# Performance work log

Hardware: AMD Instinct MI355X
Metric: run time of the kernel (lower is better)

## Reference

```python
import jax, jax.numpy as jnp
import numpy as np

HEADS = 16
DIM_HEAD = 64
SCALE = DIM_HEAD ** -0.5
LN_EPS = 1e-5


def setup_inputs() -> dict:
    key = jax.random.key(0)
    k1, k2, k3 = jax.random.split(key, 3)
    b, s, d = 2, 2048, 1024
    inner = HEADS * DIM_HEAD
    x = jax.random.normal(k1, (b, s, d), dtype=jnp.float32)
    w_qkv = jax.random.normal(k2, (d, 3 * inner), dtype=jnp.float32) * (d ** -0.5)
    w_out = jax.random.normal(k3, (inner, d), dtype=jnp.float32) * (inner ** -0.5)
    return {
        "x": x,
        "ln_gamma": jnp.ones((d,), jnp.float32),
        "ln_beta": jnp.zeros((d,), jnp.float32),
        "w_qkv": w_qkv,
        "w_out": w_out,
        "b_out": jnp.zeros((d,), jnp.float32),
    }


def _layernorm(x, gamma, beta):
    mu = jnp.mean(x, axis=-1, keepdims=True)
    var = jnp.var(x, axis=-1, keepdims=True)
    return (x - mu) * jax.lax.rsqrt(var + LN_EPS) * gamma + beta


def reference(x, ln_gamma, ln_beta, w_qkv, w_out, b_out):
    b, s, d = x.shape
    xn = _layernorm(x, ln_gamma, ln_beta)
    qkv = xn @ w_qkv                       # [b, s, 3*inner]
    q, k, v = jnp.split(qkv, 3, axis=-1)
    def heads(t):
        return t.reshape(b, s, HEADS, DIM_HEAD).transpose(0, 2, 1, 3)  # [b, h, s, dh]
    q, k, v = heads(q), heads(k), heads(v)
    dots = jnp.einsum("bhqd,bhkd->bhqk", q, k) * SCALE   # [b, h, s, s]
    attn = jax.nn.softmax(dots, axis=-1)
    out = jnp.einsum("bhqk,bhkd->bhqd", attn, v)          # [b, h, s, dh]
    out = out.transpose(0, 2, 1, 3).reshape(b, s, HEADS * DIM_HEAD)
    return out @ w_out + b_out
```

## Files before the change

### kernel.cpp

```cpp
#include <hip/hip_runtime.h>
#include <hip/hip_bf16.h>
#include <stdint.h>

#define NH     16
#define DHEAD  64
#define SEQ    2048
#define DMODEL 1024
#define NBATCH 2
#define INNER  1024
#define QKVN   3072
#define ROWS   4096
#define ATT_QB 64
#define ATT_KB 64

typedef __attribute__((ext_vector_type(8))) __bf16 bf16x8;
typedef __attribute__((ext_vector_type(4))) float floatx4;

__device__ __forceinline__ unsigned short f2bf(float f) {
    union { __bf16 b; unsigned short u; } c; c.b = (__bf16)f; return c.u;
}

__device__ __forceinline__ float fexp2(float x) {
#if __has_builtin(__builtin_amdgcn_exp2f)
    return __builtin_amdgcn_exp2f(x);
#else
    float r; asm("v_exp_f32 %0, %1" : "=v"(r) : "v"(x)); return r;
#endif
}

typedef __attribute__((address_space(1))) void gvoid;
typedef __attribute__((address_space(3))) void lvoid;
__device__ __forceinline__ void gl_lds16(const void* g, void* l) {
    __builtin_amdgcn_global_load_lds((gvoid*)g, (lvoid*)l, 16, 0, 0);
}

__global__ __launch_bounds__(256) void transpose_f2b(
        const float* __restrict__ in, unsigned short* __restrict__ out,
        int rows, int cols) {
    __shared__ unsigned short tile[32][33];
    const int bx = blockIdx.x * 32, by = blockIdx.y * 32;
    const int tx = threadIdx.x & 31, ty = threadIdx.x >> 5;
    for (int i = ty; i < 32; i += 8)
        tile[i][tx] = f2bf(in[(size_t)(by + i) * cols + bx + tx]);
    __syncthreads();
    for (int i = ty; i < 32; i += 8)
        out[(size_t)(bx + i) * rows + by + tx] = tile[tx][i];
}

__global__ __launch_bounds__(256) void ln_kernel(
        const float* __restrict__ x,
        const float* __restrict__ gamma,
        const float* __restrict__ beta,
        unsigned short* __restrict__ xn) {
    __shared__ float red[4][2];
    const int row = blockIdx.x, t = threadIdx.x;
    const size_t base = (size_t)row * DMODEL + t * 4;
    float4 v = *(const float4*)(x + base);
    float s  = v.x + v.y + v.z + v.w;
    float ss = v.x*v.x + v.y*v.y + v.z*v.z + v.w*v.w;
    for (int off = 32; off >= 1; off >>= 1) {
        s  += __shfl_xor(s,  off);
        ss += __shfl_xor(ss, off);
    }
    const int w = t >> 6, lane = t & 63;
    if (lane == 0) { red[w][0] = s; red[w][1] = ss; }
    __syncthreads();
    if (t == 0) {
        float S  = red[0][0] + red[1][0] + red[2][0] + red[3][0];
        float SS = red[0][1] + red[1][1] + red[2][1] + red[3][1];
        float mu  = S * (1.f / DMODEL);
        float var = SS * (1.f / DMODEL) - mu * mu;
        red[0][0] = mu; red[0][1] = rsqrtf(var + 1e-5f);
    }
    __syncthreads();
    const float mu = red[0][0], rstd = red[0][1];
    float4 g = *(const float4*)(gamma + t * 4);
    float4 bb = *(const float4*)(beta + t * 4);
    ushort4 o;
    o.x = f2bf((v.x - mu) * rstd * g.x + bb.x);
    o.y = f2bf((v.y - mu) * rstd * g.y + bb.y);
    o.z = f2bf((v.z - mu) * rstd * g.z + bb.z);
    o.w = f2bf((v.w - mu) * rstd * g.w + bb.w);
    *(ushort4*)(xn + base) = o;
}

__global__ __launch_bounds__(256) void gemm_qkv(
        const unsigned short* __restrict__ A,
        const unsigned short* __restrict__ Bt,
        unsigned short* __restrict__ qP,
        unsigned short* __restrict__ kP,
        unsigned short* __restrict__ vT) {
    const int K = DMODEL;
    __shared__ __align__(16) unsigned short sA[128 * 32];
    __shared__ __align__(16) unsigned short sB[128 * 32];
    __shared__ __align__(16) unsigned short tb[2][64 * 72];
    const int t = threadIdx.x;
    const int mBase = blockIdx.y * 128, nBase = blockIdx.x * 128;
    const int w = t >> 6, lane = t & 63, quad = lane >> 4, l16 = lane & 15;
    const int wm = (w >> 1) * 64, wn = (w & 1) * 64;
    const int srow = t >> 2, sch = t & 3;
    floatx4 acc[4][4];
    for (int mi = 0; mi < 4; mi++)
        for (int ni = 0; ni < 4; ni++) acc[mi][ni] = (floatx4)0.f;

    for (int k0 = 0; k0 < K; k0 += 32) {
        #pragma unroll
        for (int c = 0; c < 2; c++) {
            const int row = c * 64 + srow;
            const int gcol = (sch ^ ((row >> 1) & 3)) * 8;
            gl_lds16(&A[(size_t)(mBase + row) * K + k0 + gcol], &sA[(c * 256 + w * 64) * 8]);
            gl_lds16(&Bt[(size_t)(nBase + row) * K + k0 + gcol], &sB[(c * 256 + w * 64) * 8]);
        }
        __syncthreads();
        bf16x8 af[4], bfv[4];
        #pragma unroll
        for (int mi = 0; mi < 4; mi++) {
            const int r = wm + mi * 16 + l16;
            af[mi] = *(const bf16x8*)&sA[r * 32 + (quad ^ ((r >> 1) & 3)) * 8];
        }
        #pragma unroll
        for (int ni = 0; ni < 4; ni++) {
            const int r = wn + ni * 16 + l16;
            bfv[ni] = *(const bf16x8*)&sB[r * 32 + (quad ^ ((r >> 1) & 3)) * 8];
        }
        #pragma unroll
        for (int mi = 0; mi < 4; mi++)
            #pragma unroll
            for (int ni = 0; ni < 4; ni++)
                acc[mi][ni] = __builtin_amdgcn_mfma_f32_16x16x32_bf16(
                    af[mi], bfv[ni], acc[mi][ni], 0, 0, 0);
        __syncthreads();
    }
    const int reg = nBase >> 10;
    if (reg == 2) {
        #pragma unroll
        for (int ni = 0; ni < 4; ni++) {
            const int col = nBase + wn + ni * 16 + l16;
            const int h = (col & 1023) >> 6, dh = col & 63;
            #pragma unroll
            for (int mi = 0; mi < 4; mi++) {
                const int row0 = mBase + wm + mi * 16 + quad * 4;
                const int b = row0 >> 11, s0 = row0 & 2047;
                ushort4 o;
                o.x = f2bf(acc[mi][ni][0]); o.y = f2bf(acc[mi][ni][1]);
                o.z = f2bf(acc[mi][ni][2]); o.w = f2bf(acc[mi][ni][3]);
                *(ushort4*)&vT[((size_t)(b * NH + h) * DHEAD + dh) * SEQ + s0] = o;
            }
        }
    } else {
        unsigned short* dst = (reg == 0) ? qP : kP;
        const float scl = (reg == 0) ? 0.18033688011112042f : 1.f;
        const int hh = ((nBase + wn) & 1023) >> 6;
        #pragma unroll
        for (int ph = 0; ph < 2; ph++) {
            if ((w >> 1) == ph) {
                unsigned short* tb_ = &tb[w & 1][0];
                #pragma unroll
                for (int mi = 0; mi < 4; mi++)
                    #pragma unroll
                    for (int ni = 0; ni < 4; ni++)
                        #pragma unroll
                        for (int i = 0; i < 4; i++)
                            tb_[(mi * 16 + quad * 4 + i) * 72 + ni * 16 + l16] =
                                f2bf(acc[mi][ni][i] * scl);
                asm volatile("s_waitcnt lgkmcnt(0)" ::: "memory");
                const int row_g = mBase + wm + lane;
                const int b = row_g >> 11, sr = row_g & 2047;
                unsigned short* orow = dst + ((size_t)(b * NH + hh) * SEQ + sr) * DHEAD;
                #pragma unroll
                for (int c = 0; c < 8; c++)
                    *(bf16x8*)&orow[c * 8] = *(const bf16x8*)&tb_[lane * 72 + c * 8];
            }
            __syncthreads();
        }
    }
}

__global__ __launch_bounds__(256) void gemm_out(
        const unsigned short* __restrict__ A,
        const unsigned short* __restrict__ Bt,
        float* __restrict__ C,
        const int M, const int N, const int K,
        const float* __restrict__ bias) {
    __shared__ __align__(16) unsigned short sA[128 * 32];
    __shared__ __align__(16) unsigned short sB[64 * 32];
    const int t = threadIdx.x;
    const int mBase = blockIdx.y * 128, nBase = blockIdx.x * 64;
    const int w = t >> 6, lane = t & 63, quad = lane >> 4, l16 = lane & 15;
    const int wm = (w >> 1) * 64, wn = (w & 1) * 32;
    const int srow = t >> 2, sch = t & 3;
    floatx4 acc[4][2];
    for (int mi = 0; mi < 4; mi++)
        for (int ni = 0; ni < 2; ni++) acc[mi][ni] = (floatx4)0.f;

    for (int k0 = 0; k0 < K; k0 += 32) {
        #pragma unroll
        for (int c = 0; c < 2; c++) {
            const int row = c * 64 + srow;
            const int gcol = (sch ^ ((row >> 1) & 3)) * 8;
            gl_lds16(&A[(size_t)(mBase + row) * K + k0 + gcol], &sA[(c * 256 + w * 64) * 8]);
        }
        {
            const int gcol = (sch ^ ((srow >> 1) & 3)) * 8;
            gl_lds16(&Bt[(size_t)(nBase + srow) * K + k0 + gcol], &sB[(w * 64) * 8]);
        }
        __syncthreads();
        bf16x8 af[4], bfv[2];
        #pragma unroll
        for (int mi = 0; mi < 4; mi++) {
            const int r = wm + mi * 16 + l16;
            af[mi] = *(const bf16x8*)&sA[r * 32 + (quad ^ ((r >> 1) & 3)) * 8];
        }
        #pragma unroll
        for (int ni = 0; ni < 2; ni++) {
            const int r = wn + ni * 16 + l16;
            bfv[ni] = *(const bf16x8*)&sB[r * 32 + (quad ^ ((r >> 1) & 3)) * 8];
        }
        #pragma unroll
        for (int mi = 0; mi < 4; mi++)
            #pragma unroll
            for (int ni = 0; ni < 2; ni++)
                acc[mi][ni] = __builtin_amdgcn_mfma_f32_16x16x32_bf16(
                    af[mi], bfv[ni], acc[mi][ni], 0, 0, 0);
        __syncthreads();
    }
    #pragma unroll
    for (int mi = 0; mi < 4; mi++)
        #pragma unroll
        for (int ni = 0; ni < 2; ni++) {
            const int col = nBase + wn + ni * 16 + l16;
            const float badd = bias ? bias[col] : 0.f;
            #pragma unroll
            for (int i = 0; i < 4; i++) {
                const int row = mBase + wm + mi * 16 + quad * 4 + i;
                C[(size_t)row * N + col] = acc[mi][ni][i] + badd;
            }
        }
}

__global__ __launch_bounds__(256, 4) void attn_kernel(
        const unsigned short* __restrict__ qP,
        const unsigned short* __restrict__ kP,
        const unsigned short* __restrict__ vT,
        unsigned short* __restrict__ aout) {
    __shared__ __align__(16) unsigned short sK[2][ATT_KB * 64];
    __shared__ __align__(16) unsigned short sV[2][ATT_KB * 64];
    __shared__ __align__(16) unsigned short sP[4][16 * 64];
    const int t = threadIdx.x, w = t >> 6, lane = t & 63;
    const int quad = lane >> 4, l16 = lane & 15;
    const int bid = blockIdx.x;
    const int xcd = bid & 7, slot = bid >> 3;
    const int bh = xcd * 4 + (slot >> 5);
    const int qb = slot & 31;
    const int b = bh >> 4, h = bh & 15;
    const int qbase = qb * ATT_QB + w * 16;
    const int swr = l16 & 7;

    bf16x8 aq[2];
    #pragma unroll
    for (int hh = 0; hh < 2; hh++)
        aq[hh] = *(const bf16x8*)&qP[
            ((size_t)bh * SEQ + qbase + l16) * DHEAD + hh * 32 + quad * 8];

    floatx4 oac[4];
    float lS = 0.f;
    #pragma unroll
    for (int c = 0; c < 4; c++) oac[c] = (floatx4)0.f;

    const unsigned short* kb = kP + (size_t)bh * SEQ * DHEAD;
    const unsigned short* vb = vT + (size_t)bh * DHEAD * SEQ;
    const int r8 = lane >> 3, sw8 = ((lane & 7) ^ r8) * 8;

    auto stage = [&](int it, int bi) {
        const int kv0 = it * ATT_KB;
        #pragma unroll
        for (int ii = 0; ii < 2; ii++) {
            const int row = w * 16 + ii * 8 + r8;
            gl_lds16(kb + (size_t)(kv0 + row) * DHEAD + sw8,
                     (void*)&sK[bi][(w * 16 + ii * 8) * 64]);
            gl_lds16(vb + (size_t)row * SEQ + kv0 + sw8,
                     (void*)&sV[bi][(w * 16 + ii * 8) * 64]);
        }
    };
    stage(0, 0);

    const int NIT = SEQ / ATT_KB;
    for (int it = 0; it < NIT; ++it) {
        __syncthreads();
        if (it + 1 < NIT) stage(it + 1, (it + 1) & 1);
        const unsigned short* sKb = &sK[it & 1][0];
        const unsigned short* sVb = &sV[it & 1][0];

        bf16x8 kf[4][2];
        #pragma unroll
        for (int c = 0; c < 4; c++)
            #pragma unroll
            for (int hh = 0; hh < 2; hh++)
                kf[c][hh] = *(const bf16x8*)&sKb[(c * 16 + l16) * 64 +
                                                 8 * (((hh << 2) | quad) ^ swr)];
        floatx4 sv[4];
        __builtin_amdgcn_s_setprio(1);
        #pragma unroll
        for (int c = 0; c < 4; c++) {
            floatx4 a = (floatx4)0.f;
            a = __builtin_amdgcn_mfma_f32_16x16x32_bf16(kf[c][0], aq[0], a, 0, 0, 0);
            a = __builtin_amdgcn_mfma_f32_16x16x32_bf16(kf[c][1], aq[1], a, 0, 0, 0);
            sv[c] = a;
        }
        __builtin_amdgcn_s_setprio(0);
        {
            float sum = 0.f;
            unsigned short* pb = (unsigned short*)&sP[w][0];
            #pragma unroll
            for (int c = 0; c < 4; c++) {
                float p0 = fexp2(sv[c][0]), p1 = fexp2(sv[c][1]);
                float p2 = fexp2(sv[c][2]), p3 = fexp2(sv[c][3]);
                sum += (p0 + p1) + (p2 + p3);
                ushort4 pk;
                pk.x = f2bf(p0); pk.y = f2bf(p1); pk.z = f2bf(p2); pk.w = f2bf(p3);
                *(ushort4*)&pb[l16 * 64 + 8 * ((((c << 1) | (quad >> 1))) ^ swr) + (quad & 1) * 4] = pk;
            }
            sum += __shfl_xor(sum, 16);
            sum += __shfl_xor(sum, 32);
            lS += sum;
        }
        bf16x8 vf[4][2];
        #pragma unroll
        for (int c = 0; c < 4; c++)
            #pragma unroll
            for (int hh = 0; hh < 2; hh++)
                vf[c][hh] = *(const bf16x8*)&sVb[(c * 16 + l16) * 64 +
                                                 8 * (((hh << 2) | quad) ^ swr)];
        asm volatile("s_waitcnt lgkmcnt(0)" ::: "memory");
        {
            const unsigned short* pb = (const unsigned short*)&sP[w][0];
            bf16x8 pf[2];
            #pragma unroll
            for (int hh = 0; hh < 2; hh++)
                pf[hh] = *(const bf16x8*)&pb[l16 * 64 + 8 * (((hh << 2) | quad) ^ swr)];
            __builtin_amdgcn_s_setprio(1);
            #pragma unroll
            for (int c = 0; c < 4; c++) {
                oac[c] = __builtin_amdgcn_mfma_f32_16x16x32_bf16(vf[c][0], pf[0], oac[c], 0, 0, 0);
                oac[c] = __builtin_amdgcn_mfma_f32_16x16x32_bf16(vf[c][1], pf[1], oac[c], 0, 0, 0);
            }
            __builtin_amdgcn_s_setprio(0);
        }
    }
    const float rl = 1.f / lS;
    unsigned short* orow = aout + ((size_t)(b * SEQ + qbase + l16)) * INNER + h * DHEAD;
    #pragma unroll
    for (int c = 0; c < 4; c++) {
        ushort4 o;
        o.x = f2bf(oac[c][0] * rl);
        o.y = f2bf(oac[c][1] * rl);
        o.z = f2bf(oac[c][2] * rl);
        o.w = f2bf(oac[c][3] * rl);
        *(ushort4*)&orow[c * 16 + quad * 4] = o;
    }
}

extern "C" void kernel_launch(void* const* d_in, const int* in_sizes, int n_in,
                              void* d_out, int out_size, void* d_ws, size_t ws_size,
                              hipStream_t stream) {
    const float* x     = (const float*)d_in[0];
    const float* gamma = (const float*)d_in[1];
    const float* beta  = (const float*)d_in[2];
    const float* wqkv  = (const float*)d_in[3];
    const float* wout  = (const float*)d_in[4];
    const float* bout  = (const float*)d_in[5];
    float* out = (float*)d_out;

    unsigned short* ws     = (unsigned short*)d_ws;
    unsigned short* xn     = ws;
    unsigned short* wqkvT  = xn     + (size_t)ROWS * DMODEL;
    unsigned short* qPb    = wqkvT  + (size_t)QKVN * DMODEL;
    unsigned short* kPb    = qPb    + (size_t)NBATCH * NH * SEQ * DHEAD;
    unsigned short* vTb    = kPb    + (size_t)NBATCH * NH * SEQ * DHEAD;
    unsigned short* attnO  = vTb    + (size_t)NBATCH * NH * SEQ * DHEAD;
    unsigned short* woutT  = attnO  + (size_t)ROWS * INNER;

    transpose_f2b<<<dim3(QKVN / 32, DMODEL / 32), 256, 0, stream>>>(wqkv, wqkvT, DMODEL, QKVN);
    transpose_f2b<<<dim3(DMODEL / 32, INNER / 32), 256, 0, stream>>>(wout, woutT, INNER, DMODEL);
    ln_kernel<<<ROWS, 256, 0, stream>>>(x, gamma, beta, xn);
    gemm_qkv<<<dim3(QKVN / 128, ROWS / 128), 256, 0, stream>>>(xn, wqkvT, qPb, kPb, vTb);
    attn_kernel<<<dim3((SEQ / ATT_QB) * NBATCH * NH), 256, 0, stream>>>(
        qPb, kPb, vTb, attnO);
    gemm_out<<<dim3(DMODEL / 64, ROWS / 128), 256, 0, stream>>>(
        attnO, woutT, out, ROWS, DMODEL, INNER, bout);
}
```

Measured before the change: 216.4 us.

## Process two query sub-tiles per wave in attention with 128-thread blocks

The attention kernel now runs 2 waves per block instead of 4, and each wave handles 32 query rows as two 16-row sub-tiles. K and V fragments loaded from LDS are reused across both sub-tiles, which halves LDS fragment reads per unit of MFMA work, and each wave stages more rows of the K/V tile. The cost is higher register pressure from doubled accumulators and Q fragments, and fewer waves per block to hide latency, with launch bounds set to (128,2).

```diff
diff --git a/kernel.cpp b/kernel.cpp
--- a/kernel.cpp
+++ b/kernel.cpp
@@ -238,14 +238,14 @@
         }
 }
 
-__global__ __launch_bounds__(256, 4) void attn_kernel(
+__global__ __launch_bounds__(128, 2) void attn_kernel(
         const unsigned short* __restrict__ qP,
         const unsigned short* __restrict__ kP,
         const unsigned short* __restrict__ vT,
         unsigned short* __restrict__ aout) {
     __shared__ __align__(16) unsigned short sK[2][ATT_KB * 64];
     __shared__ __align__(16) unsigned short sV[2][ATT_KB * 64];
-    __shared__ __align__(16) unsigned short sP[4][16 * 64];
+    __shared__ __align__(16) unsigned short sP[2][2][16 * 64];
     const int t = threadIdx.x, w = t >> 6, lane = t & 63;
     const int quad = lane >> 4, l16 = lane & 15;
     const int bid = blockIdx.x;
@@ -253,19 +253,23 @@
     const int bh = xcd * 4 + (slot >> 5);
     const int qb = slot & 31;
     const int b = bh >> 4, h = bh & 15;
-    const int qbase = qb * ATT_QB + w * 16;
+    const int qbase = qb * ATT_QB + w * 32;
     const int swr = l16 & 7;
 
-    bf16x8 aq[2];
+    bf16x8 aq[2][2];
     #pragma unroll
-    for (int hh = 0; hh < 2; hh++)
-        aq[hh] = *(const bf16x8*)&qP[
-            ((size_t)bh * SEQ + qbase + l16) * DHEAD + hh * 32 + quad * 8];
-
-    floatx4 oac[4];
-    float lS = 0.f;
+    for (int st = 0; st < 2; st++)
+        #pragma unroll
+        for (int hh = 0; hh < 2; hh++)
+            aq[st][hh] = *(const bf16x8*)&qP[
+                ((size_t)bh * SEQ + qbase + st * 16 + l16) * DHEAD + hh * 32 + quad * 8];
+
+    floatx4 oac[2][4];
+    float lS[2] = {0.f, 0.f};
     #pragma unroll
-    for (int c = 0; c < 4; c++) oac[c] = (floatx4)0.f;
+    for (int st = 0; st < 2; st++)
+        #pragma unroll
+        for (int c = 0; c < 4; c++) oac[st][c] = (floatx4)0.f;
 
     const unsigned short* kb = kP + (size_t)bh * SEQ * DHEAD;
     const unsigned short* vb = vT + (size_t)bh * DHEAD * SEQ;
@@ -274,12 +278,12 @@
     auto stage = [&](int it, int bi) {
         const int kv0 = it * ATT_KB;
         #pragma unroll
-        for (int ii = 0; ii < 2; ii++) {
-            const int row = w * 16 + ii * 8 + r8;
+        for (int ii = 0; ii < 4; ii++) {
+            const int row = w * 32 + ii * 8 + r8;
             gl_lds16(kb + (size_t)(kv0 + row) * DHEAD + sw8,
-                     (void*)&sK[bi][(w * 16 + ii * 8) * 64]);
+                     (void*)&sK[bi][(w * 32 + ii * 8) * 64]);
             gl_lds16(vb + (size_t)row * SEQ + kv0 + sw8,
-                     (void*)&sV[bi][(w * 16 + ii * 8) * 64]);
+                     (void*)&sV[bi][(w * 32 + ii * 8) * 64]);
         }
     };
     stage(0, 0);
@@ -298,23 +302,26 @@
             for (int hh = 0; hh < 2; hh++)
                 kf[c][hh] = *(const bf16x8*)&sKb[(c * 16 + l16) * 64 +
                                                  8 * (((hh << 2) | quad) ^ swr)];
-        floatx4 sv[4];
+        floatx4 sv[2][4];
         __builtin_amdgcn_s_setprio(1);
         #pragma unroll
-        for (int c = 0; c < 4; c++) {
-            floatx4 a = (floatx4)0.f;
-            a = __builtin_amdgcn_mfma_f32_16x16x32_bf16(kf[c][0], aq[0], a, 0, 0, 0);
-            a = __builtin_amdgcn_mfma_f32_16x16x32_bf16(kf[c][1], aq[1], a, 0, 0, 0);
-            sv[c] = a;
-        }
+        for (int st = 0; st < 2; st++)
+            #pragma unroll
+            for (int c = 0; c < 4; c++) {
+                floatx4 a = (floatx4)0.f;
+                a = __builtin_amdgcn_mfma_f32_16x16x32_bf16(kf[c][0], aq[st][0], a, 0, 0, 0);
+                a = __builtin_amdgcn_mfma_f32_16x16x32_bf16(kf[c][1], aq[st][1], a, 0, 0, 0);
+                sv[st][c] = a;
+            }
         __builtin_amdgcn_s_setprio(0);
-        {
+        #pragma unroll
+        for (int st = 0; st < 2; st++) {
             float sum = 0.f;
-            unsigned short* pb = (unsigned short*)&sP[w][0];
+            unsigned short* pb = (unsigned short*)&sP[w][st][0];
             #pragma unroll
             for (int c = 0; c < 4; c++) {
-                float p0 = fexp2(sv[c][0]), p1 = fexp2(sv[c][1]);
-                float p2 = fexp2(sv[c][2]), p3 = fexp2(sv[c][3]);
+                float p0 = fexp2(sv[st][c][0]), p1 = fexp2(sv[st][c][1]);
+                float p2 = fexp2(sv[st][c][2]), p3 = fexp2(sv[st][c][3]);
                 sum += (p0 + p1) + (p2 + p3);
                 ushort4 pk;
                 pk.x = f2bf(p0); pk.y = f2bf(p1); pk.z = f2bf(p2); pk.w = f2bf(p3);
@@ -322,7 +329,7 @@
             }
             sum += __shfl_xor(sum, 16);
             sum += __shfl_xor(sum, 32);
-            lS += sum;
+            lS[st] += sum;
         }
         bf16x8 vf[4][2];
         #pragma unroll
@@ -332,8 +339,9 @@
                 vf[c][hh] = *(const bf16x8*)&sVb[(c * 16 + l16) * 64 +
                                                  8 * (((hh << 2) | quad) ^ swr)];
         asm volatile("s_waitcnt lgkmcnt(0)" ::: "memory");
-        {
-            const unsigned short* pb = (const unsigned short*)&sP[w][0];
+        #pragma unroll
+        for (int st = 0; st < 2; st++) {
+            const unsigned short* pb = (const unsigned short*)&sP[w][st][0];
             bf16x8 pf[2];
             #pragma unroll
             for (int hh = 0; hh < 2; hh++)
@@ -341,22 +349,26 @@
             __builtin_amdgcn_s_setprio(1);
             #pragma unroll
             for (int c = 0; c < 4; c++) {
-                oac[c] = __builtin_amdgcn_mfma_f32_16x16x32_bf16(vf[c][0], pf[0], oac[c], 0, 0, 0);
-                oac[c] = __builtin_amdgcn_mfma_f32_16x16x32_bf16(vf[c][1], pf[1], oac[c], 0, 0, 0);
+                oac[st][c] = __builtin_amdgcn_mfma_f32_16x16x32_bf16(vf[c][0], pf[0], oac[st][c], 0, 0, 0);
+                oac[st][c] = __builtin_amdgcn_mfma_f32_16x16x32_bf16(vf[c][1], pf[1], oac[st][c], 0, 0, 0);
             }
             __builtin_amdgcn_s_setprio(0);
         }
     }
-    const float rl = 1.f / lS;
-    unsigned short* orow = aout + ((size_t)(b * SEQ + qbase + l16)) * INNER + h * DHEAD;
     #pragma unroll
-    for (int c = 0; c < 4; c++) {
-        ushort4 o;
-        o.x = f2bf(oac[c][0] * rl);
-        o.y = f2bf(oac[c][1] * rl);
-        o.z = f2bf(oac[c][2] * rl);
-        o.w = f2bf(oac[c][3] * rl);
-        *(ushort4*)&orow[c * 16 + quad * 4] = o;
+    for (int st = 0; st < 2; st++) {
+        const float rl = 1.f / lS[st];
+        unsigned short* orow = aout +
+            ((size_t)(b * SEQ + qbase + st * 16 + l16)) * INNER + h * DHEAD;
+        #pragma unroll
+        for (int c = 0; c < 4; c++) {
+            ushort4 o;
+            o.x = f2bf(oac[st][c][0] * rl);
+            o.y = f2bf(oac[st][c][1] * rl);
+            o.z = f2bf(oac[st][c][2] * rl);
+            o.w = f2bf(oac[st][c][3] * rl);
+            *(ushort4*)&orow[c * 16 + quad * 4] = o;
+        }
     }
 }
 
@@ -384,7 +396,7 @@
     transpose_f2b<<<dim3(DMODEL / 32, INNER / 32), 256, 0, stream>>>(wout, woutT, INNER, DMODEL);
     ln_kernel<<<ROWS, 256, 0, stream>>>(x, gamma, beta, xn);
     gemm_qkv<<<dim3(QKVN / 128, ROWS / 128), 256, 0, stream>>>(xn, wqkvT, qPb, kPb, vTb);
-    attn_kernel<<<dim3((SEQ / ATT_QB) * NBATCH * NH), 256, 0, stream>>>(
+    attn_kernel<<<dim3((SEQ / ATT_QB) * NBATCH * NH), 128, 0, stream>>>(
         qPb, kPb, vTb, attnO);
     gemm_out<<<dim3(DMODEL / 64, ROWS / 128), 256, 0, stream>>>(
         attnO, woutT, out, ROWS, DMODEL, INNER, bout);
```

After: 217.4 us. Within noise of the previous version (+0.5%).

## Software-pipeline PV MFMA of previous tile with QK MFMA of current tile

Applied to the files above, without the earlier changes.

Restructures the attention inner loop so the P·V product for the previous KV tile is computed right after the Q·K scores for the current tile. The exp work then overlaps MFMA work instead of forming a serial chain. It adds a second barrier per iteration so the previous V buffer and sP are read before staging overwrites them, and an epilogue handles the last tile. This costs extra registers for the held V and P fragments and one more synchronisation per iteration.

```diff
diff --git a/kernel.cpp b/kernel.cpp
--- a/kernel.cpp
+++ b/kernel.cpp
@@ -287,10 +287,7 @@
     const int NIT = SEQ / ATT_KB;
     for (int it = 0; it < NIT; ++it) {
         __syncthreads();
-        if (it + 1 < NIT) stage(it + 1, (it + 1) & 1);
         const unsigned short* sKb = &sK[it & 1][0];
-        const unsigned short* sVb = &sV[it & 1][0];
-
         bf16x8 kf[4][2];
         #pragma unroll
         for (int c = 0; c < 4; c++)
@@ -298,6 +295,23 @@
             for (int hh = 0; hh < 2; hh++)
                 kf[c][hh] = *(const bf16x8*)&sKb[(c * 16 + l16) * 64 +
                                                  8 * (((hh << 2) | quad) ^ swr)];
+        bf16x8 vfp[4][2], pfp[2];
+        if (it > 0) {
+            const unsigned short* sVp = &sV[(it - 1) & 1][0];
+            #pragma unroll
+            for (int c = 0; c < 4; c++)
+                #pragma unroll
+                for (int hh = 0; hh < 2; hh++)
+                    vfp[c][hh] = *(const bf16x8*)&sVp[(c * 16 + l16) * 64 +
+                                                      8 * (((hh << 2) | quad) ^ swr)];
+            const unsigned short* pb = (const unsigned short*)&sP[w][0];
+            #pragma unroll
+            for (int hh = 0; hh < 2; hh++)
+                pfp[hh] = *(const bf16x8*)&pb[l16 * 64 + 8 * (((hh << 2) | quad) ^ swr)];
+        }
+        __syncthreads();
+        if (it + 1 < NIT) stage(it + 1, (it + 1) & 1);
+
         floatx4 sv[4];
         __builtin_amdgcn_s_setprio(1);
         #pragma unroll
@@ -307,7 +321,15 @@
             a = __builtin_amdgcn_mfma_f32_16x16x32_bf16(kf[c][1], aq[1], a, 0, 0, 0);
             sv[c] = a;
         }
+        if (it > 0) {
+            #pragma unroll
+            for (int c = 0; c < 4; c++) {
+                oac[c] = __builtin_amdgcn_mfma_f32_16x16x32_bf16(vfp[c][0], pfp[0], oac[c], 0, 0, 0);
+                oac[c] = __builtin_amdgcn_mfma_f32_16x16x32_bf16(vfp[c][1], pfp[1], oac[c], 0, 0, 0);
+            }
+        }
         __builtin_amdgcn_s_setprio(0);
+
         {
             float sum = 0.f;
             unsigned short* pb = (unsigned short*)&sP[w][0];
@@ -324,27 +346,24 @@
             sum += __shfl_xor(sum, 32);
             lS += sum;
         }
-        bf16x8 vf[4][2];
+    }
+    {
+        const unsigned short* sVp = &sV[(NIT - 1) & 1][0];
+        bf16x8 vfp[4][2], pfp[2];
         #pragma unroll
         for (int c = 0; c < 4; c++)
             #pragma unroll
             for (int hh = 0; hh < 2; hh++)
-                vf[c][hh] = *(const bf16x8*)&sVb[(c * 16 + l16) * 64 +
-                                                 8 * (((hh << 2) | quad) ^ swr)];
-        asm volatile("s_waitcnt lgkmcnt(0)" ::: "memory");
-        {
-            const unsigned short* pb = (const unsigned short*)&sP[w][0];
-            bf16x8 pf[2];
-            #pragma unroll
-            for (int hh = 0; hh < 2; hh++)
-                pf[hh] = *(const bf16x8*)&pb[l16 * 64 + 8 * (((hh << 2) | quad) ^ swr)];
-            __builtin_amdgcn_s_setprio(1);
-            #pragma unroll
-            for (int c = 0; c < 4; c++) {
-                oac[c] = __builtin_amdgcn_mfma_f32_16x16x32_bf16(vf[c][0], pf[0], oac[c], 0, 0, 0);
-                oac[c] = __builtin_amdgcn_mfma_f32_16x16x32_bf16(vf[c][1], pf[1], oac[c], 0, 0, 0);
-            }
-            __builtin_amdgcn_s_setprio(0);
+                vfp[c][hh] = *(const bf16x8*)&sVp[(c * 16 + l16) * 64 +
+                                                  8 * (((hh << 2) | quad) ^ swr)];
+        const unsigned short* pb = (const unsigned short*)&sP[w][0];
+        #pragma unroll
+        for (int hh = 0; hh < 2; hh++)
+            pfp[hh] = *(const bf16x8*)&pb[l16 * 64 + 8 * (((hh << 2) | quad) ^ swr)];
+        #pragma unroll
+        for (int c = 0; c < 4; c++) {
+            oac[c] = __builtin_amdgcn_mfma_f32_16x16x32_bf16(vfp[c][0], pfp[0], oac[c], 0, 0, 0);
+            oac[c] = __builtin_amdgcn_mfma_f32_16x16x32_bf16(vfp[c][1], pfp[1], oac[c], 0, 0, 0);
         }
     }
     const float rl = 1.f / lS;
```

Measured after the change: 213.0 us. About the same (-1.5%).
